# Kernel optimization log

Measured on AMD Instinct MI355X. Metric: run time of the kernel, lower is better.

The kernel has to match this reference:

```python
import jax, jax.numpy as jnp
import numpy as np

N = 50000      # nodes
E = 800000     # directed edges (before self-loops)
IN = 128       # input feature dim
HID = 32       # per-head hidden channels
HEADS = 4
OUT = 16       # output classes
NEG_SLOPE = 0.2


def setup_inputs() -> dict:
    key = jax.random.key(0)
    ks = jax.random.split(key, 14)
    x = jax.random.normal(ks[0], (N, IN), jnp.float32)
    edge_index = jax.random.randint(ks[1], (2, E), 0, N, dtype=jnp.int64)

    def glorot(k, shape):
        fan = shape[0] + shape[-1]
        s = np.sqrt(6.0 / fan).astype(np.float32)
        return jax.random.uniform(k, shape, jnp.float32, -s, s)

    return {
        "x": x,
        "edge_index": edge_index,
        # layer 0: IN -> HEADS*HID
        "W1": glorot(ks[2], (IN, HEADS * HID)),
        "a_src1": glorot(ks[3], (HEADS, HID)),
        "a_dst1": glorot(ks[4], (HEADS, HID)),
        "b1": jnp.zeros((HEADS * HID,), jnp.float32),
        # layer 1: HEADS*HID -> HEADS*HID
        "W2": glorot(ks[5], (HEADS * HID, HEADS * HID)),
        "a_src2": glorot(ks[6], (HEADS, HID)),
        "a_dst2": glorot(ks[7], (HEADS, HID)),
        "b2": jnp.zeros((HEADS * HID,), jnp.float32),
        # layer 2: HEADS*HID -> OUT, heads=1
        "W3": glorot(ks[8], (HEADS * HID, OUT)),
        "a_src3": glorot(ks[9], (1, OUT)),
        "a_dst3": glorot(ks[10], (1, OUT)),
        "b3": jnp.zeros((OUT,), jnp.float32),
    }


def _gat_layer(x, src, dst, W, a_s, a_d, b):
    """One PyG-style GATConv (eval mode). src/dst include self-loops."""
    H, C = a_s.shape
    h = (x @ W).reshape(N, H, C)                       # [N,H,C]
    e_src = jnp.einsum('nhc,hc->nh', h, a_s)           # [N,H]
    e_dst = jnp.einsum('nhc,hc->nh', h, a_d)
    e = jax.nn.leaky_relu(e_src[src] + e_dst[dst], NEG_SLOPE)   # [E',H]
    # segment softmax over incoming edges of each target node
    m = jax.ops.segment_max(e, dst, num_segments=N)    # [N,H]
    p = jnp.exp(e - m[dst])
    denom = jax.ops.segment_sum(p, dst, num_segments=N)
    alpha = p / (denom[dst] + 1e-16)                   # [E',H]
    out = jax.ops.segment_sum(alpha[:, :, None] * h[src], dst, num_segments=N)
    return out.reshape(N, H * C) + b


def reference(x, edge_index, W1, a_src1, a_dst1, b1, W2, a_src2, a_dst2, b2,
              W3, a_src3, a_dst3, b3):
    loops = jnp.arange(N, dtype=edge_index.dtype)
    src = jnp.concatenate([edge_index[0], loops])
    dst = jnp.concatenate([edge_index[1], loops])
    h = jax.nn.relu(_gat_layer(x, src, dst, W1, a_src1, a_dst1, b1))
    h = jax.nn.relu(_gat_layer(h, src, dst, W2, a_src2, a_dst2, b2))
    return _gat_layer(h, src, dst, W3, a_src3, a_dst3, b3)   # [N, OUT]
```

## Files before the change

### kernel.cpp

```cpp
#include <hip/hip_runtime.h>

#define NODES 50000
#define EDGES 800000
#define EPLUS (EDGES + NODES)
#define GEMMBLK 782
#define FILLBLK 3328
#define CHUNKE 2048
#define NRANGE 8
#define RSPAN 6250
#define CAP 64

typedef __attribute__((ext_vector_type(8))) short bf16x8;
typedef __attribute__((ext_vector_type(4))) float f32x4;
typedef __attribute__((ext_vector_type(4))) short short4v;

__device__ __forceinline__ float ld_f(const void* p, int isbf, size_t i) {
    if (isbf) return __uint_as_float(((unsigned)((const unsigned short*)p)[i]) << 16);
    return ((const float*)p)[i];
}
__device__ __forceinline__ int ld_idx(const int* ei, int i64, int elem) {
    int v = i64 ? ei[(size_t)elem * 2] : ei[elem];
    v = v < 0 ? 0 : v;
    return v >= NODES ? NODES - 1 : v;
}
__device__ __forceinline__ unsigned short f2bf(float f) {
    unsigned u = __float_as_uint(f);
    u = u + 0x7FFFu + ((u >> 16) & 1u);
    return (unsigned short)(u >> 16);
}
__device__ __forceinline__ unsigned pack2bf(float a, float b) {
    return (unsigned)f2bf(a) | ((unsigned)f2bf(b) << 16);
}
__device__ __forceinline__ float bflo(unsigned u) { return __uint_as_float(u << 16); }
__device__ __forceinline__ float bfhi(unsigned u) { return __uint_as_float(u & 0xFFFF0000u); }

__device__ __forceinline__ void detect_flags(const unsigned* xw, const int* eiw,
                                             int* sh, int& isbf, int& i64) {
    const int t = threadIdx.x;
    if (t < 2) sh[t] = 0;
    __syncthreads();
    if (t < 256) {
        unsigned lo = xw[t] & 0xFFFFu;
        int e = (int)((lo >> 7) & 0xFF);
        if (lo == 0u || (e >= 90 && e <= 140)) atomicAdd(&sh[0], 1);
    }
    if (t < 64) {
        if (eiw[2 * t + 1] == 0) atomicAdd(&sh[1], 1);
    }
    __syncthreads();
    isbf = sh[0] > 200 ? 1 : 0;
    i64  = sh[1] > 48 ? 1 : 0;
}

#define O_W1 0
#define O_AS1 16384
#define O_AD1 16512
#define O_B1 16640
#define O_W2 16768
#define O_AS2 33152
#define O_AD2 33280
#define O_B2 33408
#define O_W3 33536
#define O_AS3 35584
#define O_AD3 35600
#define O_B3 35616
#define W_TOTAL 35632

#define PB_CNT 196
#define PB_WC 140
#define PB_F1 64
#define PB_F2 64
#define PB_F3 8
#define PREP_GRID (PB_CNT + PB_WC + PB_F1 + PB_F2 + PB_F3)

__global__ __launch_bounds__(256) void k_prep(
        const unsigned* __restrict__ xraw, const int* __restrict__ ei,
        const void* w1, const void* as1, const void* ad1, const void* b1,
        const void* w2, const void* as2, const void* ad2, const void* b2,
        const void* w3, const void* as3, const void* ad3, const void* b3,
        float* __restrict__ Wc, int* __restrict__ cnt,
        unsigned short* __restrict__ W1fh, unsigned short* __restrict__ W1fl,
        unsigned short* __restrict__ W2fh, unsigned short* __restrict__ W2fl,
        unsigned short* __restrict__ W3fh, unsigned short* __restrict__ W3fl) {
    __shared__ int sh[2];
    const int t = threadIdx.x;
    int isbf, i64;
    detect_flags(xraw, ei, sh, isbf, i64);
    (void)i64;

    int b = blockIdx.x;
    if (b < PB_CNT) {
        int i = b * 256 + t;
        if (i < NODES) cnt[i] = 0;
        return;
    }
    b -= PB_CNT;
    if (b < PB_WC) {
        const int f = b * 256 + t;
        if (f < W_TOTAL) {
            const int sz[12] = {16384,128,128,128,16384,128,128,128,2048,16,16,16};
            const void* ps[12] = {w1,as1,ad1,b1,w2,as2,ad2,b2,w3,as3,ad3,b3};
            int off = 0;
#pragma unroll
            for (int s = 0; s < 12; ++s) {
                if (f >= off && f < off + sz[s]) Wc[f] = ld_f(ps[s], isbf, f - off);
                off += sz[s];
            }
        }
        return;
    }
    b -= PB_WC;
    const void* wsrc; unsigned short *fh, *fl; int ncols; int e;
    if (b < PB_F1)                { wsrc = w1; fh = W1fh; fl = W1fl; ncols = 128; e = b * 256 + t; }
    else if (b < PB_F1 + PB_F2)   { wsrc = w2; fh = W2fh; fl = W2fl; ncols = 128; e = (b - PB_F1) * 256 + t; }
    else                          { wsrc = w3; fh = W3fh; fl = W3fl; ncols = 16;  e = (b - PB_F1 - PB_F2) * 256 + t; }
    const int j = e & 7, l = (e >> 3) & 63;
    int nf, kc;
    if (ncols == 128) { nf = (e >> 9) & 7; kc = e >> 12; }
    else              { nf = 0;            kc = (e >> 9) & 3; }
    const int k = kc * 32 + (l >> 4) * 4 + (j & 3) + (j >> 2) * 16;
    const int n = nf * 16 + (l & 15);
    const float v = ld_f(wsrc, isbf, (size_t)k * ncols + n);
    const unsigned short hi = f2bf(v);
    const float res = v - __uint_as_float(((unsigned)hi) << 16);
    fh[e] = hi;
    fl[e] = f2bf(res);
}

__global__ __launch_bounds__(256, 4) void k_fillgemm1(
        const unsigned* __restrict__ xraw, const int* __restrict__ ei,
        const unsigned short* __restrict__ W1fh, const unsigned short* __restrict__ W1fl,
        const float* __restrict__ Wc,
        unsigned short* __restrict__ hout, float* __restrict__ es, float* __restrict__ ed,
        int* __restrict__ cnt, unsigned short* __restrict__ col) {
    __shared__ int sh[2];
    const int t = threadIdx.x;
    int isbf, i64;
    detect_flags(xraw, ei, sh, isbf, i64);

    if (blockIdx.x >= GEMMBLK) {
        const int fb = blockIdx.x - GEMMBLK;
        const int r  = blockIdx.x & 7;
        const int chunk = fb >> 3;
        const int lo = r * RSPAN, hi = lo + RSPAN;
        const int base = chunk * CHUNKE;
#pragma unroll
        for (int it = 0; it < CHUNKE / 256; ++it) {
            const int e = base + it * 256 + t;
            if (e >= EPLUS) continue;
            int s, d;
            if (e < EDGES) {
                d = ld_idx(ei, i64, EDGES + e);
                if (d < lo || d >= hi) continue;
                s = ld_idx(ei, i64, e);
            } else {
                s = d = e - EDGES;
                if (d < lo || d >= hi) continue;
            }
            int slot = atomicAdd(&cnt[d], 1);
            if (slot < CAP) col[d * CAP + slot] = (unsigned short)s;
        }
        return;
    }

    __shared__ unsigned short Ah[4 * 64 * 8];
    __shared__ unsigned short Al[4 * 64 * 8];
    const int rowBase = blockIdx.x * 64;
    const int w = t >> 6, lane = t & 63;

    f32x4 acc[4][2];
#pragma unroll
    for (int mf = 0; mf < 4; ++mf)
#pragma unroll
        for (int nn = 0; nn < 2; ++nn) acc[mf][nn] = (f32x4){0.f, 0.f, 0.f, 0.f};

    for (int kc = 0; kc < 4; ++kc) {
        __syncthreads();
#pragma unroll
        for (int u = 0; u < 2; ++u) {
            const int f = t + 256 * u;
            const int r = f >> 3, c4 = f & 7;
            int gr = rowBase + r; if (gr >= NODES) gr = NODES - 1;
            const int mf = r >> 4;
            const int l  = (r & 15) + 16 * (c4 & 3);
            const int j0 = 4 * (c4 >> 2);
            const int di = (mf * 64 + l) * 8 + j0;
            if (!isbf) {
                float4 v = *(const float4*)((const float*)xraw + (size_t)gr * 128 + kc * 32 + c4 * 4);
                const unsigned short h0 = f2bf(v.x), h1 = f2bf(v.y), h2 = f2bf(v.z), h3 = f2bf(v.w);
                short4v hv = {(short)h0, (short)h1, (short)h2, (short)h3};
                *(short4v*)&Ah[di] = hv;
                short4v lv = {(short)f2bf(v.x - __uint_as_float((unsigned)h0 << 16)),
                              (short)f2bf(v.y - __uint_as_float((unsigned)h1 << 16)),
                              (short)f2bf(v.z - __uint_as_float((unsigned)h2 << 16)),
                              (short)f2bf(v.w - __uint_as_float((unsigned)h3 << 16))};
                *(short4v*)&Al[di] = lv;
            } else {
                short4v v = *(const short4v*)((const unsigned short*)xraw + (size_t)gr * 128 + kc * 32 + c4 * 4);
                *(short4v*)&Ah[di] = v;
            }
        }
        __syncthreads();
        const int nA = 2 * w, nB = 2 * w + 1;
        const bf16x8 bh0 = *(const bf16x8*)(W1fh + (((size_t)kc * 8 + nA) * 64 + lane) * 8);
        const bf16x8 bh1 = *(const bf16x8*)(W1fh + (((size_t)kc * 8 + nB) * 64 + lane) * 8);
        const bf16x8 bl0 = *(const bf16x8*)(W1fl + (((size_t)kc * 8 + nA) * 64 + lane) * 8);
        const bf16x8 bl1 = *(const bf16x8*)(W1fl + (((size_t)kc * 8 + nB) * 64 + lane) * 8);
#pragma unroll
        for (int mf = 0; mf < 4; ++mf) {
            const bf16x8 ah = *(const bf16x8*)&Ah[(mf * 64 + lane) * 8];
            acc[mf][0] = __builtin_amdgcn_mfma_f32_16x16x32_bf16(ah, bh0, acc[mf][0], 0, 0, 0);
            acc[mf][1] = __builtin_amdgcn_mfma_f32_16x16x32_bf16(ah, bh1, acc[mf][1], 0, 0, 0);
            if (!isbf) {
                const bf16x8 al = *(const bf16x8*)&Al[(mf * 64 + lane) * 8];
                acc[mf][0] = __builtin_amdgcn_mfma_f32_16x16x32_bf16(ah, bl0, acc[mf][0], 0, 0, 0);
                acc[mf][1] = __builtin_amdgcn_mfma_f32_16x16x32_bf16(ah, bl1, acc[mf][1], 0, 0, 0);
                acc[mf][0] = __builtin_amdgcn_mfma_f32_16x16x32_bf16(al, bh0, acc[mf][0], 0, 0, 0);
                acc[mf][1] = __builtin_amdgcn_mfma_f32_16x16x32_bf16(al, bh1, acc[mf][1], 0, 0, 0);
            }
        }
    }

    const int colA = 32 * w + (lane & 15), colB = colA + 16;
    const float asA = Wc[O_AS1 + colA], asB = Wc[O_AS1 + colB];
    const float adA = Wc[O_AD1 + colA], adB = Wc[O_AD1 + colB];
    const int g = lane >> 4;
#pragma unroll
    for (int mf = 0; mf < 4; ++mf) {
#pragma unroll
        for (int r = 0; r < 4; ++r) {
            const int row = rowBase + mf * 16 + 4 * g + r;
            const bool ok = row < NODES;
            const float vA = acc[mf][0][r], vB = acc[mf][1][r];
            if (ok) {
                hout[(size_t)row * 128 + colA] = f2bf(vA);
                hout[(size_t)row * 128 + colB] = f2bf(vB);
            }
            float se = vA * asA + vB * asB;
            float sd = vA * adA + vB * adB;
#pragma unroll
            for (int off = 1; off < 16; off <<= 1) {
                se += __shfl_xor(se, off);
                sd += __shfl_xor(sd, off);
            }
            if (ok && (lane & 15) == 0) {
                es[row * 4 + w] = se;
                ed[row * 4 + w] = sd;
            }
        }
    }
}

__global__ __launch_bounds__(256, 4) void k_gemm128(
        const unsigned short* __restrict__ in,
        const unsigned short* __restrict__ Wfh, const unsigned short* __restrict__ Wfl,
        const float* __restrict__ a_s, const float* __restrict__ a_d,
        unsigned short* __restrict__ hout, float* __restrict__ es, float* __restrict__ ed) {
    __shared__ unsigned short Ah[4 * 64 * 8];
    const int t = threadIdx.x;
    const int rowBase = blockIdx.x * 64;
    const int w = t >> 6, lane = t & 63;

    f32x4 acc[4][2];
#pragma unroll
    for (int mf = 0; mf < 4; ++mf)
#pragma unroll
        for (int nn = 0; nn < 2; ++nn) acc[mf][nn] = (f32x4){0.f, 0.f, 0.f, 0.f};

    for (int kc = 0; kc < 4; ++kc) {
        __syncthreads();
#pragma unroll
        for (int u = 0; u < 2; ++u) {
            const int f = t + 256 * u;
            const int r = f >> 3, c4 = f & 7;
            int gr = rowBase + r; if (gr >= NODES) gr = NODES - 1;
            const int di = ((r >> 4) * 64 + (r & 15) + 16 * (c4 & 3)) * 8 + 4 * (c4 >> 2);
            short4v v = *(const short4v*)(in + (size_t)gr * 128 + kc * 32 + c4 * 4);
            *(short4v*)&Ah[di] = v;
        }
        __syncthreads();
        const int nA = 2 * w, nB = 2 * w + 1;
        const bf16x8 bh0 = *(const bf16x8*)(Wfh + (((size_t)kc * 8 + nA) * 64 + lane) * 8);
        const bf16x8 bh1 = *(const bf16x8*)(Wfh + (((size_t)kc * 8 + nB) * 64 + lane) * 8);
        const bf16x8 bl0 = *(const bf16x8*)(Wfl + (((size_t)kc * 8 + nA) * 64 + lane) * 8);
        const bf16x8 bl1 = *(const bf16x8*)(Wfl + (((size_t)kc * 8 + nB) * 64 + lane) * 8);
#pragma unroll
        for (int mf = 0; mf < 4; ++mf) {
            const bf16x8 ah = *(const bf16x8*)&Ah[(mf * 64 + lane) * 8];
            acc[mf][0] = __builtin_amdgcn_mfma_f32_16x16x32_bf16(ah, bh0, acc[mf][0], 0, 0, 0);
            acc[mf][1] = __builtin_amdgcn_mfma_f32_16x16x32_bf16(ah, bh1, acc[mf][1], 0, 0, 0);
            acc[mf][0] = __builtin_amdgcn_mfma_f32_16x16x32_bf16(ah, bl0, acc[mf][0], 0, 0, 0);
            acc[mf][1] = __builtin_amdgcn_mfma_f32_16x16x32_bf16(ah, bl1, acc[mf][1], 0, 0, 0);
        }
    }

    const int colA = 32 * w + (lane & 15), colB = colA + 16;
    const float asA = a_s[colA], asB = a_s[colB];
    const float adA = a_d[colA], adB = a_d[colB];
    const int g = lane >> 4;
#pragma unroll
    for (int mf = 0; mf < 4; ++mf) {
#pragma unroll
        for (int r = 0; r < 4; ++r) {
            const int row = rowBase + mf * 16 + 4 * g + r;
            const bool ok = row < NODES;
            const float vA = acc[mf][0][r], vB = acc[mf][1][r];
            if (ok) {
                hout[(size_t)row * 128 + colA] = f2bf(vA);
                hout[(size_t)row * 128 + colB] = f2bf(vB);
            }
            float se = vA * asA + vB * asB;
            float sd = vA * adA + vB * adB;
#pragma unroll
            for (int off = 1; off < 16; off <<= 1) {
                se += __shfl_xor(se, off);
                sd += __shfl_xor(sd, off);
            }
            if (ok && (lane & 15) == 0) {
                es[row * 4 + w] = se;
                ed[row * 4 + w] = sd;
            }
        }
    }
}

__global__ __launch_bounds__(256, 4) void k_gemm16(
        const unsigned short* __restrict__ in,
        const unsigned short* __restrict__ Wfh, const unsigned short* __restrict__ Wfl,
        const float* __restrict__ a_s, const float* __restrict__ a_d,
        unsigned short* __restrict__ hout, float* __restrict__ es, float* __restrict__ ed) {
    __shared__ unsigned short Ah[4 * 64 * 8];
    const int t = threadIdx.x;
    const int rowBase = blockIdx.x * 64;
    const int w = t >> 6, lane = t & 63;

    f32x4 acc = (f32x4){0.f, 0.f, 0.f, 0.f};

    for (int kc = 0; kc < 4; ++kc) {
        __syncthreads();
#pragma unroll
        for (int u = 0; u < 2; ++u) {
            const int f = t + 256 * u;
            const int r = f >> 3, c4 = f & 7;
            int gr = rowBase + r; if (gr >= NODES) gr = NODES - 1;
            const int di = ((r >> 4) * 64 + (r & 15) + 16 * (c4 & 3)) * 8 + 4 * (c4 >> 2);
            short4v v = *(const short4v*)(in + (size_t)gr * 128 + kc * 32 + c4 * 4);
            *(short4v*)&Ah[di] = v;
        }
        __syncthreads();
        const bf16x8 bh = *(const bf16x8*)(Wfh + ((size_t)kc * 64 + lane) * 8);
        const bf16x8 bl = *(const bf16x8*)(Wfl + ((size_t)kc * 64 + lane) * 8);
        const bf16x8 ah = *(const bf16x8*)&Ah[(w * 64 + lane) * 8];
        acc = __builtin_amdgcn_mfma_f32_16x16x32_bf16(ah, bh, acc, 0, 0, 0);
        acc = __builtin_amdgcn_mfma_f32_16x16x32_bf16(ah, bl, acc, 0, 0, 0);
    }

    const int c = lane & 15, g = lane >> 4;
    const float asv = a_s[c], adv = a_d[c];
#pragma unroll
    for (int r = 0; r < 4; ++r) {
        const int row = rowBase + w * 16 + 4 * g + r;
        const bool ok = row < NODES;
        if (ok) hout[(size_t)row * 16 + c] = f2bf(acc[r]);
        float se = acc[r] * asv;
        float sd = acc[r] * adv;
#pragma unroll
        for (int off = 1; off < 16; off <<= 1) {
            se += __shfl_xor(se, off);
            sd += __shfl_xor(sd, off);
        }
        if (ok && c == 0) { es[row] = se; ed[row] = sd; }
    }
}

__global__ void k_gather4(const int* __restrict__ cnt, const unsigned short* __restrict__ col,
                          const float* __restrict__ es, const float* __restrict__ ed,
                          const unsigned short* __restrict__ hfeat,
                          const float* __restrict__ bias, unsigned short* __restrict__ outb) {
    const int nd = blockIdx.x * 4 + (threadIdx.x >> 6);
    if (nd >= NODES) return;
    const int lane = threadIdx.x & 63;
    int deg = cnt[nd]; deg = deg < CAP ? deg : CAP;
    const int start = nd * CAP;

    const int esub = lane >> 4;
    const int c = lane & 15;
    const int myh = c >> 2;
    const float edh = ed[nd * 4 + myh];
    const uint4* __restrict__ h4 = (const uint4*)hfeat;
    float a[8] = {0.f,0.f,0.f,0.f,0.f,0.f,0.f,0.f};
    float den = 0.f;

    int e = esub;
    for (; e + 4 < deg; e += 8) {
        int s0 = col[start + e];
        int s1 = col[start + e + 4];
        uint4 u0 = h4[(size_t)s0 * 16 + c];
        uint4 u1 = h4[(size_t)s1 * 16 + c];
        float v0 = es[s0 * 4 + myh] + edh; v0 = v0 > 0.f ? v0 : 0.2f * v0;
        float v1 = es[s1 * 4 + myh] + edh; v1 = v1 > 0.f ? v1 : 0.2f * v1;
        float p0 = __expf(v0);
        float p1 = __expf(v1);
        den += p0 + p1;
        a[0] += p0 * bflo(u0.x) + p1 * bflo(u1.x);
        a[1] += p0 * bfhi(u0.x) + p1 * bfhi(u1.x);
        a[2] += p0 * bflo(u0.y) + p1 * bflo(u1.y);
        a[3] += p0 * bfhi(u0.y) + p1 * bfhi(u1.y);
        a[4] += p0 * bflo(u0.z) + p1 * bflo(u1.z);
        a[5] += p0 * bfhi(u0.z) + p1 * bfhi(u1.z);
        a[6] += p0 * bflo(u0.w) + p1 * bflo(u1.w);
        a[7] += p0 * bfhi(u0.w) + p1 * bfhi(u1.w);
    }
    for (; e < deg; e += 4) {
        int s0 = col[start + e];
        uint4 u0 = h4[(size_t)s0 * 16 + c];
        float v0 = es[s0 * 4 + myh] + edh; v0 = v0 > 0.f ? v0 : 0.2f * v0;
        float p0 = __expf(v0);
        den += p0;
        a[0] += p0 * bflo(u0.x);
        a[1] += p0 * bfhi(u0.x);
        a[2] += p0 * bflo(u0.y);
        a[3] += p0 * bfhi(u0.y);
        a[4] += p0 * bflo(u0.z);
        a[5] += p0 * bfhi(u0.z);
        a[6] += p0 * bflo(u0.w);
        a[7] += p0 * bfhi(u0.w);
    }
    den += __shfl_xor(den, 16);
    den += __shfl_xor(den, 32);
#pragma unroll
    for (int j = 0; j < 8; ++j) {
        a[j] += __shfl_xor(a[j], 16);
        a[j] += __shfl_xor(a[j], 32);
    }

    if (esub == 0) {
        const float inv = 1.f / (den + 1e-16f);
        float4 b0 = ((const float4*)bias)[c * 2];
        float4 b1 = ((const float4*)bias)[c * 2 + 1];
        float o0 = a[0]*inv + b0.x, o1 = a[1]*inv + b0.y;
        float o2 = a[2]*inv + b0.z, o3 = a[3]*inv + b0.w;
        float o4 = a[4]*inv + b1.x, o5 = a[5]*inv + b1.y;
        float o6 = a[6]*inv + b1.z, o7 = a[7]*inv + b1.w;
        o0 = o0 > 0.f ? o0 : 0.f;  o1 = o1 > 0.f ? o1 : 0.f;
        o2 = o2 > 0.f ? o2 : 0.f;  o3 = o3 > 0.f ? o3 : 0.f;
        o4 = o4 > 0.f ? o4 : 0.f;  o5 = o5 > 0.f ? o5 : 0.f;
        o6 = o6 > 0.f ? o6 : 0.f;  o7 = o7 > 0.f ? o7 : 0.f;
        uint4 pk = {pack2bf(o0, o1), pack2bf(o2, o3), pack2bf(o4, o5), pack2bf(o6, o7)};
        ((uint4*)outb)[(size_t)nd * 16 + c] = pk;
    }
}

__global__ void k_gather1(const int* __restrict__ cnt, const unsigned short* __restrict__ col,
                          const float* __restrict__ es, const float* __restrict__ ed,
                          const unsigned short* __restrict__ hfeat,
                          const float* __restrict__ bias, float* __restrict__ outf) {
    const int nd = blockIdx.x * 4 + (threadIdx.x >> 6);
    if (nd >= NODES) return;
    const int lane = threadIdx.x & 63;
    int deg = cnt[nd]; deg = deg < CAP ? deg : CAP;
    const int start = nd * CAP;

    const float edv = ed[nd];
    const int esub = lane >> 3;
    const int c = lane & 7;
    const unsigned* __restrict__ h1 = (const unsigned*)hfeat;
    float a0 = 0.f, a1 = 0.f, den = 0.f;

    int e = esub;
    for (; e + 8 < deg; e += 16) {
        int s0 = col[start + e];
        int s1 = col[start + e + 8];
        unsigned u0 = h1[(size_t)s0 * 8 + c];
        unsigned u1 = h1[(size_t)s1 * 8 + c];
        float v0 = es[s0] + edv; v0 = v0 > 0.f ? v0 : 0.2f * v0;
        float v1 = es[s1] + edv; v1 = v1 > 0.f ? v1 : 0.2f * v1;
        float p0 = __expf(v0);
        float p1 = __expf(v1);
        den += p0 + p1;
        a0 += p0 * bflo(u0) + p1 * bflo(u1);
        a1 += p0 * bfhi(u0) + p1 * bfhi(u1);
    }
    for (; e < deg; e += 8) {
        int s0 = col[start + e];
        unsigned u0 = h1[(size_t)s0 * 8 + c];
        float v0 = es[s0] + edv; v0 = v0 > 0.f ? v0 : 0.2f * v0;
        float p0 = __expf(v0);
        den += p0;
        a0 += p0 * bflo(u0);
        a1 += p0 * bfhi(u0);
    }
    den += __shfl_xor(den, 8);  a0 += __shfl_xor(a0, 8);  a1 += __shfl_xor(a1, 8);
    den += __shfl_xor(den, 16); a0 += __shfl_xor(a0, 16); a1 += __shfl_xor(a1, 16);
    den += __shfl_xor(den, 32); a0 += __shfl_xor(a0, 32); a1 += __shfl_xor(a1, 32);
    if (lane < 8) {
        const float inv = 1.f / (den + 1e-16f);
        float2 b = ((const float2*)bias)[c];
        ((float2*)outf)[(size_t)nd * 8 + c] = make_float2(a0 * inv + b.x, a1 * inv + b.y);
    }
}

extern "C" void kernel_launch(void* const* d_in, const int* in_sizes, int n_in,
                              void* d_out, int out_size, void* d_ws, size_t ws_size,
                              hipStream_t stream) {
    const int* ei = (const int*)d_in[1];
    const unsigned* xraw = (const unsigned*)d_in[0];
    float* out = (float*)d_out;

    char* p = (char*)d_ws;
    unsigned short* Xb  = (unsigned short*)p; p += (size_t)NODES * 128 * 2;
    unsigned short* A   = (unsigned short*)p; p += (size_t)NODES * 128 * 2;
    float*          es  = (float*)p;          p += (size_t)NODES * 4 * 4;
    float*          ed  = (float*)p;          p += (size_t)NODES * 4 * 4;
    float*          Wc  = (float*)p;          p += (size_t)W_TOTAL * 4;
    int*            cnt = (int*)p;            p += (size_t)NODES * 4;
    unsigned short* col = (unsigned short*)p; p += (size_t)NODES * CAP * 2;
    unsigned short* W1fh = (unsigned short*)p; p += 16384 * 2;
    unsigned short* W1fl = (unsigned short*)p; p += 16384 * 2;
    unsigned short* W2fh = (unsigned short*)p; p += 16384 * 2;
    unsigned short* W2fl = (unsigned short*)p; p += 16384 * 2;
    unsigned short* W3fh = (unsigned short*)p; p += 2048 * 2;
    unsigned short* W3fl = (unsigned short*)p; p += 2048 * 2;

    k_prep<<<PREP_GRID, 256, 0, stream>>>(
        xraw, ei,
        d_in[2], d_in[3], d_in[4], d_in[5],
        d_in[6], d_in[7], d_in[8], d_in[9],
        d_in[10], d_in[11], d_in[12], d_in[13],
        Wc, cnt, W1fh, W1fl, W2fh, W2fl, W3fh, W3fl);

    k_fillgemm1<<<GEMMBLK + FILLBLK, 256, 0, stream>>>(
        xraw, ei, W1fh, W1fl, Wc, A, es, ed, cnt, col);

    const int ggrid = (NODES + 3) / 4;
    k_gather4<<<ggrid, 256, 0, stream>>>(cnt, col, es, ed, A, Wc + O_B1, Xb);
    k_gemm128<<<GEMMBLK, 256, 0, stream>>>(Xb, W2fh, W2fl, Wc + O_AS2, Wc + O_AD2, A, es, ed);
    k_gather4<<<ggrid, 256, 0, stream>>>(cnt, col, es, ed, A, Wc + O_B2, Xb);
    k_gemm16<<<GEMMBLK, 256, 0, stream>>>(Xb, W3fh, W3fl, Wc + O_AS3, Wc + O_AD3, A, es, ed);
    k_gather1<<<ggrid, 256, 0, stream>>>(cnt, col, es, ed, A, Wc + O_B3, out);
}
```

Measured before the change: 253.8 us.

## Store hidden features in 16-channel slices and gather per slice

Hidden features are now stored as eight planes of 16 channels each ([8][N][16] bf16) instead of row-major [N][128]. The aggregation kernel runs one grid slice per plane, so each plane's gathered working set (about 1.6 MB) is more likely to stay in cache during the random neighbor gathers. The GEMM kernels read and write this sliced layout. It also uses nontemporal loads for x, and adds separate es/ed buffers so no kernel reads and writes the same attention-score buffer. The cost is recomputing exp and the per-edge index and score loads eight times per edge instead of four.

```diff
diff --git a/kernel.cpp b/kernel.cpp
--- a/kernel.cpp
+++ b/kernel.cpp
@@ -6,9 +6,11 @@
 #define GEMMBLK 782
 #define FILLBLK 3328
 #define CHUNKE 2048
-#define NRANGE 8
 #define RSPAN 6250
 #define CAP 64
+#define N16 (NODES * 16)
+#define GSLCH 1563
+#define GSLGRID (GSLCH * 8)
 
 typedef __attribute__((ext_vector_type(8))) short bf16x8;
 typedef __attribute__((ext_vector_type(4))) float f32x4;
@@ -27,9 +29,6 @@
     unsigned u = __float_as_uint(f);
     u = u + 0x7FFFu + ((u >> 16) & 1u);
     return (unsigned short)(u >> 16);
-}
-__device__ __forceinline__ unsigned pack2bf(float a, float b) {
-    return (unsigned)f2bf(a) | ((unsigned)f2bf(b) << 16);
 }
 __device__ __forceinline__ float bflo(unsigned u) { return __uint_as_float(u << 16); }
 __device__ __forceinline__ float bfhi(unsigned u) { return __uint_as_float(u & 0xFFFF0000u); }
@@ -131,7 +130,7 @@
         const unsigned* __restrict__ xraw, const int* __restrict__ ei,
         const unsigned short* __restrict__ W1fh, const unsigned short* __restrict__ W1fl,
         const float* __restrict__ Wc,
-        unsigned short* __restrict__ hout, float* __restrict__ es, float* __restrict__ ed,
+        unsigned short* __restrict__ hsl, float* __restrict__ es, float* __restrict__ ed,
         int* __restrict__ cnt, unsigned short* __restrict__ col) {
     __shared__ int sh[2];
     const int t = threadIdx.x;
@@ -186,17 +185,19 @@
             const int j0 = 4 * (c4 >> 2);
             const int di = (mf * 64 + l) * 8 + j0;
             if (!isbf) {
-                float4 v = *(const float4*)((const float*)xraw + (size_t)gr * 128 + kc * 32 + c4 * 4);
-                const unsigned short h0 = f2bf(v.x), h1 = f2bf(v.y), h2 = f2bf(v.z), h3 = f2bf(v.w);
+                f32x4 v = __builtin_nontemporal_load(
+                    (const f32x4*)((const float*)xraw + (size_t)gr * 128 + kc * 32 + c4 * 4));
+                const unsigned short h0 = f2bf(v[0]), h1 = f2bf(v[1]), h2 = f2bf(v[2]), h3 = f2bf(v[3]);
                 short4v hv = {(short)h0, (short)h1, (short)h2, (short)h3};
                 *(short4v*)&Ah[di] = hv;
-                short4v lv = {(short)f2bf(v.x - __uint_as_float((unsigned)h0 << 16)),
-                              (short)f2bf(v.y - __uint_as_float((unsigned)h1 << 16)),
-                              (short)f2bf(v.z - __uint_as_float((unsigned)h2 << 16)),
-                              (short)f2bf(v.w - __uint_as_float((unsigned)h3 << 16))};
+                short4v lv = {(short)f2bf(v[0] - __uint_as_float((unsigned)h0 << 16)),
+                              (short)f2bf(v[1] - __uint_as_float((unsigned)h1 << 16)),
+                              (short)f2bf(v[2] - __uint_as_float((unsigned)h2 << 16)),
+                              (short)f2bf(v[3] - __uint_as_float((unsigned)h3 << 16))};
                 *(short4v*)&Al[di] = lv;
             } else {
-                short4v v = *(const short4v*)((const unsigned short*)xraw + (size_t)gr * 128 + kc * 32 + c4 * 4);
+                short4v v = __builtin_nontemporal_load(
+                    (const short4v*)((const unsigned short*)xraw + (size_t)gr * 128 + kc * 32 + c4 * 4));
                 *(short4v*)&Ah[di] = v;
             }
         }
@@ -233,8 +234,8 @@
             const bool ok = row < NODES;
             const float vA = acc[mf][0][r], vB = acc[mf][1][r];
             if (ok) {
-                hout[(size_t)row * 128 + colA] = f2bf(vA);
-                hout[(size_t)row * 128 + colB] = f2bf(vB);
+                hsl[(size_t)(2 * w) * N16 + row * 16 + (lane & 15)]     = f2bf(vA);
+                hsl[(size_t)(2 * w + 1) * N16 + row * 16 + (lane & 15)] = f2bf(vB);
             }
             float se = vA * asA + vB * asB;
             float sd = vA * adA + vB * adB;
@@ -251,8 +252,130 @@
     }
 }
 
-__global__ __launch_bounds__(256, 4) void k_gemm128(
-        const unsigned short* __restrict__ in,
+__global__ __launch_bounds__(256, 8) void k_gsl(
+        const int* __restrict__ cnt, const unsigned short* __restrict__ col,
+        const float* __restrict__ esi, const float* __restrict__ edi,
+        const unsigned short* __restrict__ hsl, const float* __restrict__ bias,
+        unsigned short* __restrict__ xsl) {
+    const int t = threadIdx.x;
+    const int w = t >> 6, lane = t & 63;
+    const int s = blockIdx.x & 7;
+    const int chunk = blockIdx.x >> 3;
+    const int head = s >> 1;
+    const int eg = lane >> 2, cq = lane & 3;
+    const unsigned short* __restrict__ hs = hsl + (size_t)s * N16;
+    const float4 bv = *(const float4*)&bias[s * 16 + cq * 4];
+
+    for (int i = 0; i < 8; ++i) {
+        const int nd = chunk * 32 + w * 8 + i;
+        if (nd >= NODES) break;
+        int deg = cnt[nd]; deg = deg < CAP ? deg : CAP;
+        const int start = nd * CAP;
+        const float edh = edi[nd * 4 + head];
+        float a0 = 0.f, a1 = 0.f, a2 = 0.f, a3 = 0.f, den = 0.f;
+        for (int e = eg; e < deg; e += 16) {
+            int s0 = col[start + e];
+            uint2 u = *(const uint2*)&hs[s0 * 16 + cq * 4];
+            float v = esi[s0 * 4 + head] + edh; v = v > 0.f ? v : 0.2f * v;
+            float p = __expf(v);
+            den += p;
+            a0 += p * bflo(u.x); a1 += p * bfhi(u.x);
+            a2 += p * bflo(u.y); a3 += p * bfhi(u.y);
+        }
+#pragma unroll
+        for (int off = 4; off < 64; off <<= 1) {
+            den += __shfl_xor(den, off);
+            a0 += __shfl_xor(a0, off); a1 += __shfl_xor(a1, off);
+            a2 += __shfl_xor(a2, off); a3 += __shfl_xor(a3, off);
+        }
+        if (lane < 4) {
+            const float inv = 1.f / (den + 1e-16f);
+            float o0 = a0 * inv + bv.x, o1 = a1 * inv + bv.y;
+            float o2 = a2 * inv + bv.z, o3 = a3 * inv + bv.w;
+            o0 = o0 > 0.f ? o0 : 0.f;  o1 = o1 > 0.f ? o1 : 0.f;
+            o2 = o2 > 0.f ? o2 : 0.f;  o3 = o3 > 0.f ? o3 : 0.f;
+            short4v pk = {(short)f2bf(o0), (short)f2bf(o1), (short)f2bf(o2), (short)f2bf(o3)};
+            *(short4v*)&xsl[(size_t)s * N16 + nd * 16 + lane * 4] = pk;
+        }
+    }
+}
+
+__global__ __launch_bounds__(256, 4) void k_gemm2(
+        const unsigned short* __restrict__ xsl,
+        const unsigned short* __restrict__ Wfh, const unsigned short* __restrict__ Wfl,
+        const float* __restrict__ a_s, const float* __restrict__ a_d,
+        unsigned short* __restrict__ hsl, float* __restrict__ es, float* __restrict__ ed) {
+    __shared__ unsigned short Ah[4 * 64 * 8];
+    const int t = threadIdx.x;
+    const int rowBase = blockIdx.x * 64;
+    const int w = t >> 6, lane = t & 63;
+
+    f32x4 acc[4][2];
+#pragma unroll
+    for (int mf = 0; mf < 4; ++mf)
+#pragma unroll
+        for (int nn = 0; nn < 2; ++nn) acc[mf][nn] = (f32x4){0.f, 0.f, 0.f, 0.f};
+
+    for (int kc = 0; kc < 4; ++kc) {
+        __syncthreads();
+#pragma unroll
+        for (int u = 0; u < 2; ++u) {
+            const int f = t + 256 * u;
+            const int r = f >> 3, c4 = f & 7;
+            int gr = rowBase + r; if (gr >= NODES) gr = NODES - 1;
+            const int di = ((r >> 4) * 64 + (r & 15) + 16 * (c4 & 3)) * 8 + 4 * (c4 >> 2);
+            const int ch0 = kc * 32 + c4 * 4;
+            short4v v = *(const short4v*)&xsl[(size_t)(ch0 >> 4) * N16 + gr * 16 + (ch0 & 15)];
+            *(short4v*)&Ah[di] = v;
+        }
+        __syncthreads();
+        const int nA = 2 * w, nB = 2 * w + 1;
+        const bf16x8 bh0 = *(const bf16x8*)(Wfh + (((size_t)kc * 8 + nA) * 64 + lane) * 8);
+        const bf16x8 bh1 = *(const bf16x8*)(Wfh + (((size_t)kc * 8 + nB) * 64 + lane) * 8);
+        const bf16x8 bl0 = *(const bf16x8*)(Wfl + (((size_t)kc * 8 + nA) * 64 + lane) * 8);
+        const bf16x8 bl1 = *(const bf16x8*)(Wfl + (((size_t)kc * 8 + nB) * 64 + lane) * 8);
+#pragma unroll
+        for (int mf = 0; mf < 4; ++mf) {
+            const bf16x8 ah = *(const bf16x8*)&Ah[(mf * 64 + lane) * 8];
+            acc[mf][0] = __builtin_amdgcn_mfma_f32_16x16x32_bf16(ah, bh0, acc[mf][0], 0, 0, 0);
+            acc[mf][1] = __builtin_amdgcn_mfma_f32_16x16x32_bf16(ah, bh1, acc[mf][1], 0, 0, 0);
+            acc[mf][0] = __builtin_amdgcn_mfma_f32_16x16x32_bf16(ah, bl0, acc[mf][0], 0, 0, 0);
+            acc[mf][1] = __builtin_amdgcn_mfma_f32_16x16x32_bf16(ah, bl1, acc[mf][1], 0, 0, 0);
+        }
+    }
+
+    const int colA = 32 * w + (lane & 15), colB = colA + 16;
+    const float asA = a_s[colA], asB = a_s[colB];
+    const float adA = a_d[colA], adB = a_d[colB];
+    const int g = lane >> 4;
+#pragma unroll
+    for (int mf = 0; mf < 4; ++mf) {
+#pragma unroll
+        for (int r = 0; r < 4; ++r) {
+            const int row = rowBase + mf * 16 + 4 * g + r;
+            const bool ok = row < NODES;
+            const float vA = acc[mf][0][r], vB = acc[mf][1][r];
+            if (ok) {
+                hsl[(size_t)(2 * w) * N16 + row * 16 + (lane & 15)]     = f2bf(vA);
+                hsl[(size_t)(2 * w + 1) * N16 + row * 16 + (lane & 15)] = f2bf(vB);
+            }
+            float se = vA * asA + vB * asB;
+            float sd = vA * adA + vB * adB;
+#pragma unroll
+            for (int off = 1; off < 16; off <<= 1) {
+                se += __shfl_xor(se, off);
+                sd += __shfl_xor(sd, off);
+            }
+            if (ok && (lane & 15) == 0) {
+                es[row * 4 + w] = se;
+                ed[row * 4 + w] = sd;
+            }
+        }
+    }
+}
+
+__global__ __launch_bounds__(256, 4) void k_gemm3(
+        const unsigned short* __restrict__ xsl,
         const unsigned short* __restrict__ Wfh, const unsigned short* __restrict__ Wfl,
         const float* __restrict__ a_s, const float* __restrict__ a_d,
         unsigned short* __restrict__ hout, float* __restrict__ es, float* __restrict__ ed) {
@@ -261,11 +384,7 @@
     const int rowBase = blockIdx.x * 64;
     const int w = t >> 6, lane = t & 63;
 
-    f32x4 acc[4][2];
-#pragma unroll
-    for (int mf = 0; mf < 4; ++mf)
-#pragma unroll
-        for (int nn = 0; nn < 2; ++nn) acc[mf][nn] = (f32x4){0.f, 0.f, 0.f, 0.f};
+    f32x4 acc = (f32x4){0.f, 0.f, 0.f, 0.f};
 
     for (int kc = 0; kc < 4; ++kc) {
         __syncthreads();
@@ -275,76 +394,8 @@
             const int r = f >> 3, c4 = f & 7;
             int gr = rowBase + r; if (gr >= NODES) gr = NODES - 1;
             const int di = ((r >> 4) * 64 + (r & 15) + 16 * (c4 & 3)) * 8 + 4 * (c4 >> 2);
-            short4v v = *(const short4v*)(in + (size_t)gr * 128 + kc * 32 + c4 * 4);
-            *(short4v*)&Ah[di] = v;
-        }
-        __syncthreads();
-        const int nA = 2 * w, nB = 2 * w + 1;
-        const bf16x8 bh0 = *(const bf16x8*)(Wfh + (((size_t)kc * 8 + nA) * 64 + lane) * 8);
-        const bf16x8 bh1 = *(const bf16x8*)(Wfh + (((size_t)kc * 8 + nB) * 64 + lane) * 8);
-        const bf16x8 bl0 = *(const bf16x8*)(Wfl + (((size_t)kc * 8 + nA) * 64 + lane) * 8);
-        const bf16x8 bl1 = *(const bf16x8*)(Wfl + (((size_t)kc * 8 + nB) * 64 + lane) * 8);
-#pragma unroll
-        for (int mf = 0; mf < 4; ++mf) {
-            const bf16x8 ah = *(const bf16x8*)&Ah[(mf * 64 + lane) * 8];
-            acc[mf][0] = __builtin_amdgcn_mfma_f32_16x16x32_bf16(ah, bh0, acc[mf][0], 0, 0, 0);
-            acc[mf][1] = __builtin_amdgcn_mfma_f32_16x16x32_bf16(ah, bh1, acc[mf][1], 0, 0, 0);
-            acc[mf][0] = __builtin_amdgcn_mfma_f32_16x16x32_bf16(ah, bl0, acc[mf][0], 0, 0, 0);
-            acc[mf][1] = __builtin_amdgcn_mfma_f32_16x16x32_bf16(ah, bl1, acc[mf][1], 0, 0, 0);
-        }
-    }
-
-    const int colA = 32 * w + (lane & 15), colB = colA + 16;
-    const float asA = a_s[colA], asB = a_s[colB];
-    const float adA = a_d[colA], adB = a_d[colB];
-    const int g = lane >> 4;
-#pragma unroll
-    for (int mf = 0; mf < 4; ++mf) {
-#pragma unroll
-        for (int r = 0; r < 4; ++r) {
-            const int row = rowBase + mf * 16 + 4 * g + r;
-            const bool ok = row < NODES;
-            const float vA = acc[mf][0][r], vB = acc[mf][1][r];
-            if (ok) {
-                hout[(size_t)row * 128 + colA] = f2bf(vA);
-                hout[(size_t)row * 128 + colB] = f2bf(vB);
-            }
-            float se = vA * asA + vB * asB;
-            float sd = vA * adA + vB * adB;
-#pragma unroll
-            for (int off = 1; off < 16; off <<= 1) {
-                se += __shfl_xor(se, off);
-                sd += __shfl_xor(sd, off);
-            }
-            if (ok && (lane & 15) == 0) {
-                es[row * 4 + w] = se;
-                ed[row * 4 + w] = sd;
-            }
-        }
-    }
-}
-
-__global__ __launch_bounds__(256, 4) void k_gemm16(
-        const unsigned short* __restrict__ in,
-        const unsigned short* __restrict__ Wfh, const unsigned short* __restrict__ Wfl,
-        const float* __restrict__ a_s, const float* __restrict__ a_d,
-        unsigned short* __restrict__ hout, float* __restrict__ es, float* __restrict__ ed) {
-    __shared__ unsigned short Ah[4 * 64 * 8];
-    const int t = threadIdx.x;
-    const int rowBase = blockIdx.x * 64;
-    const int w = t >> 6, lane = t & 63;
-
-    f32x4 acc = (f32x4){0.f, 0.f, 0.f, 0.f};
-
-    for (int kc = 0; kc < 4; ++kc) {
-        __syncthreads();
-#pragma unroll
-        for (int u = 0; u < 2; ++u) {
-            const int f = t + 256 * u;
-            const int r = f >> 3, c4 = f & 7;
-            int gr = rowBase + r; if (gr >= NODES) gr = NODES - 1;
-            const int di = ((r >> 4) * 64 + (r & 15) + 16 * (c4 & 3)) * 8 + 4 * (c4 >> 2);
-            short4v v = *(const short4v*)(in + (size_t)gr * 128 + kc * 32 + c4 * 4);
+            const int ch0 = kc * 32 + c4 * 4;
+            short4v v = *(const short4v*)&xsl[(size_t)(ch0 >> 4) * N16 + gr * 16 + (ch0 & 15)];
             *(short4v*)&Ah[di] = v;
         }
         __syncthreads();
@@ -370,84 +421,6 @@
             sd += __shfl_xor(sd, off);
         }
         if (ok && c == 0) { es[row] = se; ed[row] = sd; }
-    }
-}
-
-__global__ void k_gather4(const int* __restrict__ cnt, const unsigned short* __restrict__ col,
-                          const float* __restrict__ es, const float* __restrict__ ed,
-                          const unsigned short* __restrict__ hfeat,
-                          const float* __restrict__ bias, unsigned short* __restrict__ outb) {
-    const int nd = blockIdx.x * 4 + (threadIdx.x >> 6);
-    if (nd >= NODES) return;
-    const int lane = threadIdx.x & 63;
-    int deg = cnt[nd]; deg = deg < CAP ? deg : CAP;
-    const int start = nd * CAP;
-
-    const int esub = lane >> 4;
-    const int c = lane & 15;
-    const int myh = c >> 2;
-    const float edh = ed[nd * 4 + myh];
-    const uint4* __restrict__ h4 = (const uint4*)hfeat;
-    float a[8] = {0.f,0.f,0.f,0.f,0.f,0.f,0.f,0.f};
-    float den = 0.f;
-
-    int e = esub;
-    for (; e + 4 < deg; e += 8) {
-        int s0 = col[start + e];
-        int s1 = col[start + e + 4];
-        uint4 u0 = h4[(size_t)s0 * 16 + c];
-        uint4 u1 = h4[(size_t)s1 * 16 + c];
-        float v0 = es[s0 * 4 + myh] + edh; v0 = v0 > 0.f ? v0 : 0.2f * v0;
-        float v1 = es[s1 * 4 + myh] + edh; v1 = v1 > 0.f ? v1 : 0.2f * v1;
-        float p0 = __expf(v0);
-        float p1 = __expf(v1);
-        den += p0 + p1;
-        a[0] += p0 * bflo(u0.x) + p1 * bflo(u1.x);
-        a[1] += p0 * bfhi(u0.x) + p1 * bfhi(u1.x);
-        a[2] += p0 * bflo(u0.y) + p1 * bflo(u1.y);
-        a[3] += p0 * bfhi(u0.y) + p1 * bfhi(u1.y);
-        a[4] += p0 * bflo(u0.z) + p1 * bflo(u1.z);
-        a[5] += p0 * bfhi(u0.z) + p1 * bfhi(u1.z);
-        a[6] += p0 * bflo(u0.w) + p1 * bflo(u1.w);
-        a[7] += p0 * bfhi(u0.w) + p1 * bfhi(u1.w);
-    }
-    for (; e < deg; e += 4) {
-        int s0 = col[start + e];
-        uint4 u0 = h4[(size_t)s0 * 16 + c];
-        float v0 = es[s0 * 4 + myh] + edh; v0 = v0 > 0.f ? v0 : 0.2f * v0;
-        float p0 = __expf(v0);
-        den += p0;
-        a[0] += p0 * bflo(u0.x);
-        a[1] += p0 * bfhi(u0.x);
-        a[2] += p0 * bflo(u0.y);
-        a[3] += p0 * bfhi(u0.y);
-        a[4] += p0 * bflo(u0.z);
-        a[5] += p0 * bfhi(u0.z);
-        a[6] += p0 * bflo(u0.w);
-        a[7] += p0 * bfhi(u0.w);
-    }
-    den += __shfl_xor(den, 16);
-    den += __shfl_xor(den, 32);
-#pragma unroll
-    for (int j = 0; j < 8; ++j) {
-        a[j] += __shfl_xor(a[j], 16);
-        a[j] += __shfl_xor(a[j], 32);
-    }
-
-    if (esub == 0) {
-        const float inv = 1.f / (den + 1e-16f);
-        float4 b0 = ((const float4*)bias)[c * 2];
-        float4 b1 = ((const float4*)bias)[c * 2 + 1];
-        float o0 = a[0]*inv + b0.x, o1 = a[1]*inv + b0.y;
-        float o2 = a[2]*inv + b0.z, o3 = a[3]*inv + b0.w;
-        float o4 = a[4]*inv + b1.x, o5 = a[5]*inv + b1.y;
-        float o6 = a[6]*inv + b1.z, o7 = a[7]*inv + b1.w;
-        o0 = o0 > 0.f ? o0 : 0.f;  o1 = o1 > 0.f ? o1 : 0.f;
-        o2 = o2 > 0.f ? o2 : 0.f;  o3 = o3 > 0.f ? o3 : 0.f;
-        o4 = o4 > 0.f ? o4 : 0.f;  o5 = o5 > 0.f ? o5 : 0.f;
-        o6 = o6 > 0.f ? o6 : 0.f;  o7 = o7 > 0.f ? o7 : 0.f;
-        uint4 pk = {pack2bf(o0, o1), pack2bf(o2, o3), pack2bf(o4, o5), pack2bf(o6, o7)};
-        ((uint4*)outb)[(size_t)nd * 16 + c] = pk;
     }
 }
 
@@ -508,10 +481,10 @@
     float* out = (float*)d_out;
 
     char* p = (char*)d_ws;
-    unsigned short* Xb  = (unsigned short*)p; p += (size_t)NODES * 128 * 2;
-    unsigned short* A   = (unsigned short*)p; p += (size_t)NODES * 128 * 2;
-    float*          es  = (float*)p;          p += (size_t)NODES * 4 * 4;
-    float*          ed  = (float*)p;          p += (size_t)NODES * 4 * 4;
+    unsigned short* bufA = (unsigned short*)p; p += (size_t)NODES * 128 * 2;
+    unsigned short* bufB = (unsigned short*)p; p += (size_t)NODES * 128 * 2;
+    float*          es1 = (float*)p;          p += (size_t)NODES * 4 * 4;
+    float*          ed1 = (float*)p;          p += (size_t)NODES * 4 * 4;
     float*          Wc  = (float*)p;          p += (size_t)W_TOTAL * 4;
     int*            cnt = (int*)p;            p += (size_t)NODES * 4;
     unsigned short* col = (unsigned short*)p; p += (size_t)NODES * CAP * 2;
@@ -521,6 +494,8 @@
     unsigned short* W2fl = (unsigned short*)p; p += 16384 * 2;
     unsigned short* W3fh = (unsigned short*)p; p += 2048 * 2;
     unsigned short* W3fl = (unsigned short*)p; p += 2048 * 2;
+    float*          es2 = (float*)p;          p += (size_t)NODES * 4 * 4;
+    float*          ed2 = (float*)p;          p += (size_t)NODES * 4 * 4;
 
     k_prep<<<PREP_GRID, 256, 0, stream>>>(
         xraw, ei,
@@ -530,12 +505,16 @@
         Wc, cnt, W1fh, W1fl, W2fh, W2fl, W3fh, W3fl);
 
     k_fillgemm1<<<GEMMBLK + FILLBLK, 256, 0, stream>>>(
-        xraw, ei, W1fh, W1fl, Wc, A, es, ed, cnt, col);
+        xraw, ei, W1fh, W1fl, Wc, bufA, es1, ed1, cnt, col);
+
+    k_gsl<<<GSLGRID, 256, 0, stream>>>(cnt, col, es1, ed1, bufA, Wc + O_B1, bufB);
+    k_gemm2<<<GEMMBLK, 256, 0, stream>>>(bufB, W2fh, W2fl, Wc + O_AS2, Wc + O_AD2,
+                                         bufA, es2, ed2);
+
+    k_gsl<<<GSLGRID, 256, 0, stream>>>(cnt, col, es2, ed2, bufA, Wc + O_B2, bufB);
+    k_gemm3<<<GEMMBLK, 256, 0, stream>>>(bufB, W3fh, W3fl, Wc + O_AS3, Wc + O_AD3,
+                                         bufA, es1, ed1);
 
     const int ggrid = (NODES + 3) / 4;
-    k_gather4<<<ggrid, 256, 0, stream>>>(cnt, col, es, ed, A, Wc + O_B1, Xb);
-    k_gemm128<<<GEMMBLK, 256, 0, stream>>>(Xb, W2fh, W2fl, Wc + O_AS2, Wc + O_AD2, A, es, ed);
-    k_gather4<<<ggrid, 256, 0, stream>>>(cnt, col, es, ed, A, Wc + O_B2, Xb);
-    k_gemm16<<<GEMMBLK, 256, 0, stream>>>(Xb, W3fh, W3fl, Wc + O_AS3, Wc + O_AD3, A, es, ed);
-    k_gather1<<<ggrid, 256, 0, stream>>>(cnt, col, es, ed, A, Wc + O_B3, out);
-}
+    k_gather1<<<ggrid, 256, 0, stream>>>(cnt, col, es1, ed1, bufA, Wc + O_B3, out);
+}
```

New measurement: 387.3 us. 52.6% more time.
